# Kernel tuning notes

Hardware: AMD Instinct MI355X
Metric: run time of the kernel (lower is better)

## Reference

```python
import jax, jax.numpy as jnp
import numpy as np

B, N, D_IN, D, K, H, ITERS = 128, 4096, 64, 64, 8, 128, 3
SCALE = D ** -0.5
EPS_ATTN = 1e-8
EPS_LN = 1e-5


def layer_norm(x, g, b):
    m = jnp.mean(x, axis=-1, keepdims=True)
    v = jnp.mean((x - m) ** 2, axis=-1, keepdims=True)
    return (x - m) * jax.lax.rsqrt(v + EPS_LN) * g + b


def setup_inputs() -> dict:
    key = jax.random.key(0)
    ks = jax.random.split(key, 16)
    s = 0.05
    return {
        "inputs": jax.random.normal(ks[0], (B, N, D_IN), dtype=jnp.float32),
        "noise": jax.random.normal(ks[1], (B, K, D), dtype=jnp.float32),
        "slots_mu": jax.random.normal(ks[2], (1, 1, D), dtype=jnp.float32),
        "slots_sigma": jax.random.normal(ks[3], (1, 1, D), dtype=jnp.float32),
        "Wq": jax.random.normal(ks[4], (D, D), dtype=jnp.float32) * s,
        "Wk": jax.random.normal(ks[5], (D_IN, D), dtype=jnp.float32) * s,
        "Wv": jax.random.normal(ks[6], (D_IN, D), dtype=jnp.float32) * s,
        "W_ih": jax.random.normal(ks[7], (3 * D, D), dtype=jnp.float32) * s,
        "W_hh": jax.random.normal(ks[8], (3 * D, D), dtype=jnp.float32) * s,
        "b_ih": jnp.zeros((3 * D,), dtype=jnp.float32),
        "b_hh": jnp.zeros((3 * D,), dtype=jnp.float32),
        "mlp_W1": jax.random.normal(ks[9], (D, H), dtype=jnp.float32) * s,
        "mlp_b1": jnp.zeros((H,), dtype=jnp.float32),
        "mlp_W2": jax.random.normal(ks[10], (H, D), dtype=jnp.float32) * s,
        "mlp_b2": jnp.zeros((D,), dtype=jnp.float32),
        "ln_in_g": jnp.ones((D_IN,), dtype=jnp.float32),
        "ln_in_b": jnp.zeros((D_IN,), dtype=jnp.float32),
        "ln_s_g": jnp.ones((D,), dtype=jnp.float32),
        "ln_s_b": jnp.zeros((D,), dtype=jnp.float32),
        "ln_ff_g": jnp.ones((D,), dtype=jnp.float32),
        "ln_ff_b": jnp.zeros((D,), dtype=jnp.float32),
    }


def reference(inputs, noise, slots_mu, slots_sigma, Wq, Wk, Wv,
              W_ih, W_hh, b_ih, b_hh, mlp_W1, mlp_b1, mlp_W2, mlp_b2,
              ln_in_g, ln_in_b, ln_s_g, ln_s_b, ln_ff_g, ln_ff_b):
    # slots = Normal(mu, sigma) with externally supplied standard noise
    slots = slots_mu + slots_sigma * noise                      # [B,K,D]
    x = layer_norm(inputs, ln_in_g, ln_in_b)                     # [B,N,D_IN]
    k = x @ Wk                                                   # [B,N,D]
    v = x @ Wv                                                   # [B,N,D]

    for _ in range(ITERS):
        slots_prev = slots
        s = layer_norm(slots, ln_s_g, ln_s_b)
        q = s @ Wq                                               # [B,K,D]
        dots = jnp.einsum('bid,bjd->bij', q, k) * SCALE          # [B,K,N]
        attn = jax.nn.softmax(dots, axis=1) + EPS_ATTN           # softmax over slots
        attn_n = attn / jnp.sum(attn, axis=-1, keepdims=True)
        updates = jnp.einsum('bjd,bij->bid', v, attn_n)          # [B,K,D]

        # single-step GRU (torch nn.GRU gate order: reset, update, new)
        gx = updates @ W_ih.T + b_ih                             # [B,K,3D]
        gh = slots_prev @ W_hh.T + b_hh                          # [B,K,3D]
        gx_r, gx_z, gx_n = jnp.split(gx, 3, axis=-1)
        gh_r, gh_z, gh_n = jnp.split(gh, 3, axis=-1)
        r = jax.nn.sigmoid(gx_r + gh_r)
        z = jax.nn.sigmoid(gx_z + gh_z)
        n = jnp.tanh(gx_n + r * gh_n)
        slots = (1.0 - z) * n + z * slots_prev

        slots = layer_norm(slots, ln_ff_g, ln_ff_b)
        slots = slots + (jax.nn.relu(slots @ mlp_W1 + mlp_b1) @ mlp_W2 + mlp_b2)
    return slots
```

## Files before the change

kernel.cpp:

```cpp
#include <hip/hip_runtime.h>
#include <hip/hip_bf16.h>

typedef unsigned int u32;
typedef unsigned short u16;
typedef __attribute__((ext_vector_type(8))) short short8;
typedef __attribute__((ext_vector_type(4))) float f32x4;
typedef __attribute__((ext_vector_type(2))) u32 u32x2;

#define B_      128
#define N_      4096
#define K_      8
#define SCALE_  0.125f
#define EPS_A   1e-8f
#define EPS_LN  1e-5f

__device__ __forceinline__ float bf_lo(u32 u){ union{u32 v; float f;} x; x.v = u<<16; return x.f; }
__device__ __forceinline__ u16 f2bf(float f){
  union{float f; u32 v;} x; x.f = f;
  u32 v = x.v;
  return (u16)((v + 0x7fffu + ((v>>16)&1u))>>16);
}
__device__ __forceinline__ float wsum64(float v){
  #pragma unroll
  for (int off=32; off; off>>=1) v += __shfl_xor(v, off, 64);
  return v;
}
__device__ __forceinline__ void gll16(const void* g, void* l){
  __builtin_amdgcn_global_load_lds(
      (const __attribute__((address_space(1))) void*)g,
      (__attribute__((address_space(3))) void*)l, 16, 0, 0);
}

__global__ void prep_t(const float* __restrict__ Wih, const float* __restrict__ Whh,
                       const float* __restrict__ Wq,  const float* __restrict__ Wk,
                       float* __restrict__ WihT, float* __restrict__ WhhT,
                       float* __restrict__ Wqk, int* __restrict__ flags){
  int t = threadIdx.x;
  if (blockIdx.x == 0 && t < B_) flags[t] = 0;
  if (blockIdx.x < 48){
    int idx = blockIdx.x*256 + t;
    int g = idx>>6, d = idx&63;
    WihT[d*192+g] = Wih[idx];
    WhhT[d*192+g] = Whh[idx];
  } else {
    __shared__ float WkL[64*65];
    int bi = blockIdx.x - 48;
    #pragma unroll
    for (int k=0;k<16;++k){
      int idx = t + k*256;
      int d = idx>>6, m = idx&63;
      WkL[m*65+d] = Wk[idx];
    }
    __syncthreads();
    int a = bi*4 + (t>>6), d = t&63;
    float acc = 0.f;
    #pragma unroll 8
    for (int m=0;m<64;++m) acc += Wq[a*64+m]*WkL[m*65+d];
    Wqk[a*64+d] = acc;
  }
}

__device__ __forceinline__ void tile_attn(
    char* ibuf, char* abuf, short8 qf0, short8 qf1,
    int fr, int fq, f32x4* c2, float* tsl)
{
  f32x4 c1[2];
  #pragma unroll
  for (int nt=0;nt<2;++nt){
    c1[nt] = (f32x4){0.f,0.f,0.f,0.f};
    #pragma unroll
    for (int kk=0;kk<2;++kk){
      int byte = ((kk*2+(fq>>1))<<10) | (((fr>>2)&1)<<9)
               | ((nt*2+(fr>>3))<<7) | ((fr&3)<<5) | ((fq&1)<<4);
      short8 xf = *(const short8*)(ibuf + byte);
      c1[nt] = __builtin_amdgcn_mfma_f32_16x16x32_bf16(kk?qf1:qf0, xf, c1[nt], 0,0,0);
    }
  }
  #pragma unroll
  for (int nt=0;nt<2;++nt){
    float d0 = c1[nt][0]*SCALE_, d1 = c1[nt][1]*SCALE_;
    float d2 = c1[nt][2]*SCALE_, d3 = c1[nt][3]*SCALE_;
    float m = fmaxf(fmaxf(d0,d1), fmaxf(d2,d3));
    m = fmaxf(m, __shfl_xor(m, 16, 64));
    float e0 = __expf(d0-m), e1 = __expf(d1-m), e2 = __expf(d2-m), e3 = __expf(d3-m);
    float sl = e0+e1+e2+e3;
    float inv = 1.f/(sl + __shfl_xor(sl, 16, 64));
    float a0 = e0*inv + EPS_A, a1 = e1*inv + EPS_A;
    float a2 = e2*inv + EPS_A, a3 = e3*inv + EPS_A;
    tsl[0]+=a0; tsl[1]+=a1; tsl[2]+=a2; tsl[3]+=a3;
    int pos2 = (nt*16 + fr)*2;
    *(u16*)(abuf + (((fq*4+0)*64 + pos2) ^ (0<<4))) = f2bf(a0);
    *(u16*)(abuf + (((fq*4+1)*64 + pos2) ^ (1<<4))) = f2bf(a1);
    *(u16*)(abuf + (((fq*4+2)*64 + pos2) ^ (2<<4))) = f2bf(a2);
    *(u16*)(abuf + (((fq*4+3)*64 + pos2) ^ (3<<4))) = f2bf(a3);
  }
  asm volatile("s_waitcnt lgkmcnt(0)" ::: "memory");
  __builtin_amdgcn_sched_barrier(0);
  {
    short8 pa = *(const short8*)(abuf + ((fr*64 + fq*16) ^ ((fr&3)<<4)));
    u32 va = (u32)(size_t)ibuf + (fq<<7) + (fr<<1);
    u32x2 tv0,tv1,tv2,tv3,tv4,tv5,tv6,tv7;
    asm volatile("ds_read_b64_tr_b16 %0, %1 offset:0"    : "=v"(tv0) : "v"(va));
    asm volatile("ds_read_b64_tr_b16 %0, %1 offset:512"  : "=v"(tv1) : "v"(va));
    asm volatile("ds_read_b64_tr_b16 %0, %1 offset:1024" : "=v"(tv2) : "v"(va));
    asm volatile("ds_read_b64_tr_b16 %0, %1 offset:1536" : "=v"(tv3) : "v"(va));
    asm volatile("ds_read_b64_tr_b16 %0, %1 offset:2048" : "=v"(tv4) : "v"(va));
    asm volatile("ds_read_b64_tr_b16 %0, %1 offset:2560" : "=v"(tv5) : "v"(va));
    asm volatile("ds_read_b64_tr_b16 %0, %1 offset:3072" : "=v"(tv6) : "v"(va));
    asm volatile("ds_read_b64_tr_b16 %0, %1 offset:3584" : "=v"(tv7) : "v"(va));
    asm volatile("s_waitcnt lgkmcnt(0)" ::: "memory");
    __builtin_amdgcn_sched_barrier(0);
    union { short8 s8; u32 u4[4]; } xb;
    xb.u4[0]=tv0.x; xb.u4[1]=tv0.y; xb.u4[2]=tv1.x; xb.u4[3]=tv1.y;
    c2[0] = __builtin_amdgcn_mfma_f32_16x16x32_bf16(pa, xb.s8, c2[0], 0,0,0);
    xb.u4[0]=tv2.x; xb.u4[1]=tv2.y; xb.u4[2]=tv3.x; xb.u4[3]=tv3.y;
    c2[1] = __builtin_amdgcn_mfma_f32_16x16x32_bf16(pa, xb.s8, c2[1], 0,0,0);
    xb.u4[0]=tv4.x; xb.u4[1]=tv4.y; xb.u4[2]=tv5.x; xb.u4[3]=tv5.y;
    c2[2] = __builtin_amdgcn_mfma_f32_16x16x32_bf16(pa, xb.s8, c2[2], 0,0,0);
    xb.u4[0]=tv6.x; xb.u4[1]=tv6.y; xb.u4[2]=tv7.x; xb.u4[3]=tv7.y;
    c2[3] = __builtin_amdgcn_mfma_f32_16x16x32_bf16(pa, xb.s8, c2[3], 0,0,0);
  }
}

__global__ __launch_bounds__(512,1) void fused_sa(
    const float* __restrict__ inp, u16* __restrict__ xhat,
    const float* __restrict__ noise, const float* __restrict__ mu, const float* __restrict__ sigma,
    const float* __restrict__ Wqk,
    const float* __restrict__ lng, const float* __restrict__ lnb,
    const float* __restrict__ lnsg, const float* __restrict__ lnsb,
    const float* __restrict__ WihT, const float* __restrict__ WhhT,
    const float* __restrict__ bih, const float* __restrict__ bhh,
    const float* __restrict__ W1, const float* __restrict__ b1,
    const float* __restrict__ W2, const float* __restrict__ b2,
    const float* __restrict__ lnffg, const float* __restrict__ lnffb,
    const float* __restrict__ Wv,
    float* __restrict__ PUg, float* __restrict__ PSg, int* __restrict__ flags,
    float* __restrict__ dout)
{
  __shared__ __align__(16) char smem[152320];
  int bid = blockIdx.x, t = threadIdx.x;
  int b = bid & 127, half = bid >> 7;
  int w = t>>6, lane = t&63;
  int fr = lane&15, fq = lane>>4;
  int i = w, d = lane;

  char*  wbase = smem + w*9216;
  char*  abuf  = wbase + 8192;
  char*  qA    = smem + 73728;
  float* UL    = (float*)(smem + 75776);
  float* SL    = (float*)(smem + 92160);
  u16*   wih_l = (u16*)(smem + 92416);
  u16*   whh_l = (u16*)(smem + 116992);
  float* updL  = (float*)(smem + 141568);
  float* spL   = (float*)(smem + 143744);
  float* sfL   = (float*)(smem + 145920);
  float* hL    = (float*)(smem + 148096);

  {
    const float4* wa = (const float4*)WihT;
    const float4* wb = (const float4*)WhhT;
    #pragma unroll
    for (int k2=0;k2<6;++k2){
      int idx = t + k2*512;
      float4 va = wa[idx], vb = wb[idx];
      ((u32*)wih_l)[idx*2]   = (u32)f2bf(va.x) | ((u32)f2bf(va.y)<<16);
      ((u32*)wih_l)[idx*2+1] = (u32)f2bf(va.z) | ((u32)f2bf(va.w)<<16);
      ((u32*)whh_l)[idx*2]   = (u32)f2bf(vb.x) | ((u32)f2bf(vb.y)<<16);
      ((u32*)whh_l)[idx*2+1] = (u32)f2bf(vb.z) | ((u32)f2bf(vb.w)<<16);
    }
  }
  if (t < 256) ((u32*)(qA + 1024))[t] = 0;
  float sp = mu[d] + sigma[d]*noise[b*512 + t];
  {
    float m  = wsum64(sp)*(1.f/64.f);
    float df = sp - m;
    float vv = wsum64(df*df)*(1.f/64.f);
    float sv = df*rsqrtf(vv+EPS_LN)*lnsg[d] + lnsb[d];
    updL[i*68+d] = sv;
  }
  __syncthreads();
  {
    float qt = 0.f;
    #pragma unroll 8
    for (int dd=0; dd<64; ++dd) qt += updL[i*68+dd]*Wqk[dd*64 + d];
    *(u16*)(qA + ((i*128 + d*2) ^ ((i&7)<<4))) = f2bf(qt);
  }
  __syncthreads();

  long tbase = (long)b*128 + half*64 + w*8;

  for (int it=0; it<3; ++it){
    f32x4 c2[4];
    #pragma unroll
    for (int k2=0;k2<4;++k2) c2[k2] = (f32x4){0.f,0.f,0.f,0.f};
    float tsl[4] = {0.f,0.f,0.f,0.f};
    short8 qf0 = *(const short8*)(qA + ((fr*128 +  0 + fq*16) ^ ((fr&7)<<4)));
    short8 qf1 = *(const short8*)(qA + ((fr*128 + 64 + fq*16) ^ ((fr&7)<<4)));

    if (it == 0){
      for (int tile=0; tile<8; ++tile){
        char* ibuf = wbase;
        {
          int r = lane>>1, hx = lane&1;
          const float4* xr = (const float4*)(inp +
              ((long)b*N_ + half*2048 + w*256 + tile*32 + r)*64 + hx*32);
          float xv[32]; float s=0.f, sq=0.f;
          #pragma unroll
          for (int c=0;c<8;++c){
            float4 f = xr[c];
            xv[c*4+0]=f.x; xv[c*4+1]=f.y; xv[c*4+2]=f.z; xv[c*4+3]=f.w;
            s  += f.x+f.y+f.z+f.w;
            sq += f.x*f.x+f.y*f.y+f.z*f.z+f.w*f.w;
          }
          s  += __shfl_xor(s,1,64);
          sq += __shfl_xor(sq,1,64);
          float mean = s*(1.f/64.f);
          float inv  = rsqrtf(sq*(1.f/64.f) - mean*mean + EPS_LN);
          float lgv[32], lbv[32];
          {
            const float4* g4 = (const float4*)(lng + hx*32);
            const float4* b4 = (const float4*)(lnb + hx*32);
            #pragma unroll
            for (int e=0;e<8;++e){
              float4 gv = g4[e], bv = b4[e];
              lgv[e*4+0]=gv.x; lgv[e*4+1]=gv.y; lgv[e*4+2]=gv.z; lgv[e*4+3]=gv.w;
              lbv[e*4+0]=bv.x; lbv[e*4+1]=bv.y; lbv[e*4+2]=bv.z; lbv[e*4+3]=bv.w;
            }
          }
          u32 pk[16];
          #pragma unroll
          for (int e=0;e<16;++e){
            float a0 = (xv[e*2]  -mean)*inv*lgv[e*2]   + lbv[e*2];
            float a1 = (xv[e*2+1]-mean)*inv*lgv[e*2+1] + lbv[e*2+1];
            pk[e] = (u32)f2bf(a0) | ((u32)f2bf(a1)<<16);
          }
          int pbits = (((r>>2)&1)<<9) | (((r>>3)&3)<<7) | ((r&3)<<5);
          #pragma unroll
          for (int hf=0; hf<2; ++hf){
            int dt = hx*2 + hf;
            uint4 v0; v0.x=pk[hf*8+0]; v0.y=pk[hf*8+1]; v0.z=pk[hf*8+2]; v0.w=pk[hf*8+3];
            uint4 v1; v1.x=pk[hf*8+4]; v1.y=pk[hf*8+5]; v1.z=pk[hf*8+6]; v1.w=pk[hf*8+7];
            *(uint4*)(ibuf + ((dt<<10) | pbits))      = v0;
            *(uint4*)(ibuf + ((dt<<10) | pbits) + 16) = v1;
          }
          asm volatile("s_waitcnt lgkmcnt(0)" ::: "memory");
          __builtin_amdgcn_sched_barrier(0);
          char* gim = (char*)xhat + ((tbase+tile)<<12) + lane*16;
          #pragma unroll
          for (int j=0;j<4;++j)
            *(uint4*)(gim + j*1024) = *(const uint4*)(ibuf + lane*16 + j*1024);
        }
        tile_attn(ibuf, abuf, qf0, qf1, fr, fq, c2, tsl);
      }
      asm volatile("s_waitcnt vmcnt(0)" ::: "memory");
      __builtin_amdgcn_sched_barrier(0);
    } else {
      {
        const char* g0 = (const char*)xhat + (tbase<<12) + lane*16;
        #pragma unroll
        for (int j=0;j<4;++j) gll16(g0 + j*1024, wbase + j*1024);
      }
      #pragma unroll 2
      for (int tile=0; tile<8; ++tile){
        char* ibuf = wbase + (tile&1)*4096;
        if (tile < 7){
          const char* gn = (const char*)xhat + ((tbase+tile+1)<<12) + lane*16;
          char* ln = wbase + ((tile+1)&1)*4096;
          #pragma unroll
          for (int j=0;j<4;++j) gll16(gn + j*1024, ln + j*1024);
          asm volatile("s_waitcnt vmcnt(4)" ::: "memory");
        } else {
          asm volatile("s_waitcnt vmcnt(0)" ::: "memory");
        }
        __builtin_amdgcn_sched_barrier(0);
        tile_attn(ibuf, abuf, qf0, qf1, fr, fq, c2, tsl);
      }
    }
    if (fq < 2){
      #pragma unroll
      for (int dblk=0;dblk<4;++dblk){
        #pragma unroll
        for (int r2=0;r2<4;++r2)
          UL[w*512 + (fq*4+r2)*64 + dblk*16 + fr] = c2[dblk][r2];
      }
    }
    #pragma unroll
    for (int mk=1; mk<16; mk<<=1){
      tsl[0] += __shfl_xor(tsl[0], mk, 64);
      tsl[1] += __shfl_xor(tsl[1], mk, 64);
      tsl[2] += __shfl_xor(tsl[2], mk, 64);
      tsl[3] += __shfl_xor(tsl[3], mk, 64);
    }
    if (fr==0 && fq<2){
      SL[w*8 + fq*4+0] = tsl[0]; SL[w*8 + fq*4+1] = tsl[1];
      SL[w*8 + fq*4+2] = tsl[2]; SL[w*8 + fq*4+3] = tsl[3];
    }
    __syncthreads();

    float u = 0.f, S = 0.f;
    #pragma unroll
    for (int cw=0; cw<8; ++cw){
      u += UL[cw*512 + i*64 + d];
      S += SL[cw*8 + i];
    }
    {
      long pbase = ((long)it*256 + bid);
      __hip_atomic_store(&PUg[pbase*512 + t], u, __ATOMIC_RELAXED, __HIP_MEMORY_SCOPE_AGENT);
      if (d == 0)
        __hip_atomic_store(&PSg[pbase*8 + i], S, __ATOMIC_RELAXED, __HIP_MEMORY_SCOPE_AGENT);
    }
    asm volatile("s_waitcnt vmcnt(0)" ::: "memory");
    __syncthreads();
    if (t == 0){
      __hip_atomic_fetch_add(&flags[b], 1, __ATOMIC_RELAXED, __HIP_MEMORY_SCOPE_AGENT);
      while (__hip_atomic_load(&flags[b], __ATOMIC_RELAXED, __HIP_MEMORY_SCOPE_AGENT) < 2*(it+1))
        __builtin_amdgcn_s_sleep(2);
    }
    __syncthreads();
    {
      long obase = ((long)it*256 + (bid ^ 128));
      u += __hip_atomic_load(&PUg[obase*512 + t], __ATOMIC_RELAXED, __HIP_MEMORY_SCOPE_AGENT);
      S += __hip_atomic_load(&PSg[obase*8 + i], __ATOMIC_RELAXED, __HIP_MEMORY_SCOPE_AGENT);
    }

    float ut = u / S;
    sfL[i*68+d] = ut;
    spL[i*68+d] = sp;
    __syncthreads();
    float upd = 0.f;
    #pragma unroll 8
    for (int dd=0; dd<64; ++dd) upd += sfL[i*68+dd]*Wv[dd*64 + d];
    updL[i*68+d] = upd;
    __syncthreads();
    float gx0 = bih[d], gx1 = bih[64+d], gx2 = bih[128+d];
    float gh0 = bhh[d], gh1 = bhh[64+d], gh2 = bhh[128+d];
    #pragma unroll 8
    for (int dd=0; dd<64; ++dd){
      float uv = updL[i*68+dd];
      float sv = spL[i*68+dd];
      gx0 += uv*bf_lo((u32)wih_l[dd*192 + d]);
      gx1 += uv*bf_lo((u32)wih_l[dd*192 + 64 + d]);
      gx2 += uv*bf_lo((u32)wih_l[dd*192 + 128 + d]);
      gh0 += sv*bf_lo((u32)whh_l[dd*192 + d]);
      gh1 += sv*bf_lo((u32)whh_l[dd*192 + 64 + d]);
      gh2 += sv*bf_lo((u32)whh_l[dd*192 + 128 + d]);
    }
    float rg = 1.f/(1.f+__expf(-(gx0+gh0)));
    float zg = 1.f/(1.f+__expf(-(gx1+gh1)));
    float ng = tanhf(gx2 + rg*gh2);
    float sn = (1.f-zg)*ng + zg*sp;
    float m1 = wsum64(sn)*(1.f/64.f);
    float df = sn-m1;
    float vv = wsum64(df*df)*(1.f/64.f);
    float sf = df*rsqrtf(vv+EPS_LN)*lnffg[d] + lnffb[d];
    sfL[i*68+d] = sf;
    __syncthreads();
    float h0 = b1[d], h1 = b1[64+d];
    #pragma unroll 8
    for (int dd=0;dd<64;++dd){
      float sv = sfL[i*68+dd];
      h0 += sv*W1[dd*128 + d];
      h1 += sv*W1[dd*128 + 64 + d];
    }
    h0 = fmaxf(h0, 0.f); h1 = fmaxf(h1, 0.f);
    hL[i*132+d] = h0; hL[i*132+64+d] = h1;
    __syncthreads();
    float o = b2[d];
    #pragma unroll 8
    for (int hh=0; hh<128; ++hh) o += hL[i*132+hh]*W2[hh*64 + d];
    float out = sf + o;
    sp = out;
    if (it == 2){
      if (half == 0) dout[b*512 + t] = out;
    } else {
      float m2 = wsum64(out)*(1.f/64.f);
      float d2 = out-m2;
      float v2 = wsum64(d2*d2)*(1.f/64.f);
      float sq = d2*rsqrtf(v2+EPS_LN)*lnsg[d] + lnsb[d];
      updL[i*68+d] = sq;
      __syncthreads();
      float qt = 0.f;
      #pragma unroll 8
      for (int dd=0;dd<64;++dd) qt += updL[i*68+dd]*Wqk[dd*64 + d];
      *(u16*)(qA + ((i*128 + d*2) ^ ((i&7)<<4))) = f2bf(qt);
      __syncthreads();
    }
  }
}

extern "C" void kernel_launch(void* const* d_in, const int* in_sizes, int n_in,
                              void* d_out, int out_size, void* d_ws, size_t ws_size,
                              hipStream_t stream){
  const float* inp   = (const float*)d_in[0];
  const float* noise = (const float*)d_in[1];
  const float* mu    = (const float*)d_in[2];
  const float* sigma = (const float*)d_in[3];
  const float* Wq    = (const float*)d_in[4];
  const float* Wk    = (const float*)d_in[5];
  const float* Wv    = (const float*)d_in[6];
  const float* Wih   = (const float*)d_in[7];
  const float* Whh   = (const float*)d_in[8];
  const float* bih   = (const float*)d_in[9];
  const float* bhh   = (const float*)d_in[10];
  const float* W1    = (const float*)d_in[11];
  const float* b1    = (const float*)d_in[12];
  const float* W2    = (const float*)d_in[13];
  const float* b2    = (const float*)d_in[14];
  const float* lnig  = (const float*)d_in[15];
  const float* lnib  = (const float*)d_in[16];
  const float* lnsg  = (const float*)d_in[17];
  const float* lnsb  = (const float*)d_in[18];
  const float* lnffg = (const float*)d_in[19];
  const float* lnffb = (const float*)d_in[20];
  float* out = (float*)d_out;

  char* ws = (char*)d_ws;
  u16*   xhat  = (u16*)(ws);
  float* WihT  = (float*)(ws + 67108864);
  float* WhhT  = (float*)(ws + 67158016);
  float* Wqk   = (float*)(ws + 67207168);
  float* PUg   = (float*)(ws + 67223552);
  float* PSg   = (float*)(ws + 68796416);
  int*   flags = (int*)(ws + 68820992);

  prep_t<<<64,256,0,stream>>>(Wih, Whh, Wq, Wk, WihT, WhhT, Wqk, flags);
  fused_sa<<<2*B_,512,0,stream>>>(inp, xhat, noise, mu, sigma, Wqk,
                                  lnig, lnib, lnsg, lnsb,
                                  WihT, WhhT, bih, bhh,
                                  W1, b1, W2, b2, lnffg, lnffb, Wv,
                                  PUg, PSg, flags, out);
}
```

Baseline: 130.2 us.

## Widen per-wave LDS staging to two tiles and stream GRU weights through aliased LDS

Each wave's LDS area grows from two 4KB tile buffers to two 8KB buffers, so two xhat tiles are prefetched and consumed per pipeline step. That halves the number of wait points and deepens the global_load_lds prefetch. To free the space, the persistent bf16 GRU weight copies are removed. W_ih and W_hh are now reloaded as fp32 from global into an aliased region once per iteration, and the per-slot scratch buffers alias the wave tile areas. This adds global weight reload traffic and extra barriers each iteration, but drops the bf16 rounding of the GRU weights.

```diff
diff --git a/kernel.cpp b/kernel.cpp
--- a/kernel.cpp
+++ b/kernel.cpp
@@ -10,6 +10,7 @@
 #define B_      128
 #define N_      4096
 #define K_      8
+#define AREA    17408
 #define SCALE_  0.125f
 #define EPS_A   1e-8f
 #define EPS_LN  1e-5f
@@ -137,38 +138,23 @@
     float* __restrict__ PUg, float* __restrict__ PSg, int* __restrict__ flags,
     float* __restrict__ dout)
 {
-  __shared__ __align__(16) char smem[152320];
+  __shared__ __align__(16) char smem[141568];
   int bid = blockIdx.x, t = threadIdx.x;
   int b = bid & 127, half = bid >> 7;
   int w = t>>6, lane = t&63;
   int fr = lane&15, fq = lane>>4;
   int i = w, d = lane;
 
-  char*  wbase = smem + w*9216;
-  char*  abuf  = wbase + 8192;
-  char*  qA    = smem + 73728;
-  float* UL    = (float*)(smem + 75776);
-  float* SL    = (float*)(smem + 92160);
-  u16*   wih_l = (u16*)(smem + 92416);
-  u16*   whh_l = (u16*)(smem + 116992);
-  float* updL  = (float*)(smem + 141568);
-  float* spL   = (float*)(smem + 143744);
-  float* sfL   = (float*)(smem + 145920);
-  float* hL    = (float*)(smem + 148096);
-
-  {
-    const float4* wa = (const float4*)WihT;
-    const float4* wb = (const float4*)WhhT;
-    #pragma unroll
-    for (int k2=0;k2<6;++k2){
-      int idx = t + k2*512;
-      float4 va = wa[idx], vb = wb[idx];
-      ((u32*)wih_l)[idx*2]   = (u32)f2bf(va.x) | ((u32)f2bf(va.y)<<16);
-      ((u32*)wih_l)[idx*2+1] = (u32)f2bf(va.z) | ((u32)f2bf(va.w)<<16);
-      ((u32*)whh_l)[idx*2]   = (u32)f2bf(vb.x) | ((u32)f2bf(vb.y)<<16);
-      ((u32*)whh_l)[idx*2+1] = (u32)f2bf(vb.z) | ((u32)f2bf(vb.w)<<16);
-    }
-  }
+  char*  wbase = smem + w*AREA;
+  char*  abuf  = wbase + 16384;
+  char*  qA    = smem + 139264;
+  float* SLp   = (float*)(smem + 141312);
+  float* updL  = (float*)(smem + 0*AREA + 4096);
+  float* spL   = (float*)(smem + 1*AREA + 4096);
+  float* sfL   = (float*)(smem + 2*AREA + 4096);
+  float* hL    = (float*)(smem + 3*AREA + 4096);
+  float* wls   = (float*)(smem + 4*AREA);
+
   if (t < 256) ((u32*)(qA + 1024))[t] = 0;
   float sp = mu[d] + sigma[d]*noise[b*512 + t];
   {
@@ -257,51 +243,56 @@
     } else {
       {
         const char* g0 = (const char*)xhat + (tbase<<12) + lane*16;
+        char* ln = wbase;
         #pragma unroll
-        for (int j=0;j<4;++j) gll16(g0 + j*1024, wbase + j*1024);
-      }
-      #pragma unroll 2
-      for (int tile=0; tile<8; ++tile){
-        char* ibuf = wbase + (tile&1)*4096;
-        if (tile < 7){
-          const char* gn = (const char*)xhat + ((tbase+tile+1)<<12) + lane*16;
-          char* ln = wbase + ((tile+1)&1)*4096;
-          #pragma unroll
-          for (int j=0;j<4;++j) gll16(gn + j*1024, ln + j*1024);
-          asm volatile("s_waitcnt vmcnt(4)" ::: "memory");
+        for (int j=0;j<8;++j) gll16(g0 + j*1024, ln + j*1024);
+      }
+      #pragma unroll
+      for (int p=0; p<4; ++p){
+        char* pb = wbase + (p&1)*8192;
+        if (p < 3){
+          const char* gn = (const char*)xhat + ((tbase + (long)(p+1)*2)<<12) + lane*16;
+          char* ln = wbase + ((p+1)&1)*8192;
+          #pragma unroll
+          for (int j=0;j<8;++j) gll16(gn + j*1024, ln + j*1024);
+          asm volatile("s_waitcnt vmcnt(8)" ::: "memory");
         } else {
           asm volatile("s_waitcnt vmcnt(0)" ::: "memory");
         }
         __builtin_amdgcn_sched_barrier(0);
-        tile_attn(ibuf, abuf, qf0, qf1, fr, fq, c2, tsl);
-      }
-    }
-    if (fq < 2){
+        tile_attn(pb,        abuf, qf0, qf1, fr, fq, c2, tsl);
+        tile_attn(pb + 4096, abuf, qf0, qf1, fr, fq, c2, tsl);
+      }
+    }
+    {
+      float* ULw = (float*)wbase;
+      if (fq < 2){
+        #pragma unroll
+        for (int dblk=0;dblk<4;++dblk){
+          #pragma unroll
+          for (int r2=0;r2<4;++r2)
+            ULw[(fq*4+r2)*64 + dblk*16 + fr] = c2[dblk][r2];
+        }
+      }
       #pragma unroll
-      for (int dblk=0;dblk<4;++dblk){
-        #pragma unroll
-        for (int r2=0;r2<4;++r2)
-          UL[w*512 + (fq*4+r2)*64 + dblk*16 + fr] = c2[dblk][r2];
-      }
-    }
-    #pragma unroll
-    for (int mk=1; mk<16; mk<<=1){
-      tsl[0] += __shfl_xor(tsl[0], mk, 64);
-      tsl[1] += __shfl_xor(tsl[1], mk, 64);
-      tsl[2] += __shfl_xor(tsl[2], mk, 64);
-      tsl[3] += __shfl_xor(tsl[3], mk, 64);
-    }
-    if (fr==0 && fq<2){
-      SL[w*8 + fq*4+0] = tsl[0]; SL[w*8 + fq*4+1] = tsl[1];
-      SL[w*8 + fq*4+2] = tsl[2]; SL[w*8 + fq*4+3] = tsl[3];
+      for (int mk=1; mk<16; mk<<=1){
+        tsl[0] += __shfl_xor(tsl[0], mk, 64);
+        tsl[1] += __shfl_xor(tsl[1], mk, 64);
+        tsl[2] += __shfl_xor(tsl[2], mk, 64);
+        tsl[3] += __shfl_xor(tsl[3], mk, 64);
+      }
+      if (fr==0 && fq<2){
+        SLp[w*8 + fq*4+0] = tsl[0]; SLp[w*8 + fq*4+1] = tsl[1];
+        SLp[w*8 + fq*4+2] = tsl[2]; SLp[w*8 + fq*4+3] = tsl[3];
+      }
     }
     __syncthreads();
 
     float u = 0.f, S = 0.f;
     #pragma unroll
     for (int cw=0; cw<8; ++cw){
-      u += UL[cw*512 + i*64 + d];
-      S += SL[cw*8 + i];
+      u += ((const float*)(smem + cw*AREA))[i*64 + d];
+      S += SLp[cw*8 + i];
     }
     {
       long pbase = ((long)it*256 + bid);
@@ -327,23 +318,38 @@
     sfL[i*68+d] = ut;
     spL[i*68+d] = sp;
     __syncthreads();
+    {
+      const float4* wa = (const float4*)WihT;
+      #pragma unroll
+      for (int k2=0;k2<6;++k2){ int idx = t + k2*512; ((float4*)wls)[idx] = wa[idx]; }
+    }
     float upd = 0.f;
     #pragma unroll 8
     for (int dd=0; dd<64; ++dd) upd += sfL[i*68+dd]*Wv[dd*64 + d];
     updL[i*68+d] = upd;
     __syncthreads();
     float gx0 = bih[d], gx1 = bih[64+d], gx2 = bih[128+d];
-    float gh0 = bhh[d], gh1 = bhh[64+d], gh2 = bhh[128+d];
     #pragma unroll 8
     for (int dd=0; dd<64; ++dd){
       float uv = updL[i*68+dd];
+      gx0 += uv*wls[dd*192 + d];
+      gx1 += uv*wls[dd*192 + 64 + d];
+      gx2 += uv*wls[dd*192 + 128 + d];
+    }
+    __syncthreads();
+    {
+      const float4* wb = (const float4*)WhhT;
+      #pragma unroll
+      for (int k2=0;k2<6;++k2){ int idx = t + k2*512; ((float4*)wls)[idx] = wb[idx]; }
+    }
+    __syncthreads();
+    float gh0 = bhh[d], gh1 = bhh[64+d], gh2 = bhh[128+d];
+    #pragma unroll 8
+    for (int dd=0; dd<64; ++dd){
       float sv = spL[i*68+dd];
-      gx0 += uv*bf_lo((u32)wih_l[dd*192 + d]);
-      gx1 += uv*bf_lo((u32)wih_l[dd*192 + 64 + d]);
-      gx2 += uv*bf_lo((u32)wih_l[dd*192 + 128 + d]);
-      gh0 += sv*bf_lo((u32)whh_l[dd*192 + d]);
-      gh1 += sv*bf_lo((u32)whh_l[dd*192 + 64 + d]);
-      gh2 += sv*bf_lo((u32)whh_l[dd*192 + 128 + d]);
+      gh0 += sv*wls[dd*192 + d];
+      gh1 += sv*wls[dd*192 + 64 + d];
+      gh2 += sv*wls[dd*192 + 128 + d];
     }
     float rg = 1.f/(1.f+__expf(-(gx0+gh0)));
     float zg = 1.f/(1.f+__expf(-(gx1+gh1)));
@@ -353,6 +359,7 @@
     float df = sn-m1;
     float vv = wsum64(df*df)*(1.f/64.f);
     float sf = df*rsqrtf(vv+EPS_LN)*lnffg[d] + lnffb[d];
+    __syncthreads();
     sfL[i*68+d] = sf;
     __syncthreads();
     float h0 = b1[d], h1 = b1[64+d];
```

Measured after the change: 152.2 us. 16.9% more time.
